# Performance work log

Measured on AMD Instinct MI355X. Metric: run time of the kernel, lower is better.

The kernel has to match this reference:

```python
import jax, jax.numpy as jnp
import numpy as np

N, K, D = 1000000, 4, 16

def setup_inputs() -> dict:
    key = jax.random.key(0)
    k1, k2, k3, k4, k5 = jax.random.split(key, 5)
    z = jax.random.normal(k1, (N, D), dtype=jnp.float32)
    phi = jax.nn.softmax(jax.random.normal(k2, (K,), dtype=jnp.float32))  # mixture weights, sum to 1
    mu = jax.random.normal(k3, (K, D), dtype=jnp.float32)
    # Upper-triangular Cholesky-like factor with positive diagonal (module calls
    # solve_triangular(..., upper=True), i.e. L is treated as upper triangular).
    A = jax.random.normal(k4, (K, D, D), dtype=jnp.float32) * 0.1
    diag = 0.8 + 0.4 * jax.random.uniform(k5, (K, D), dtype=jnp.float32)
    L = jnp.triu(A, 1) + jnp.zeros((K, D, D), jnp.float32).at[:, jnp.arange(D), jnp.arange(D)].set(diag)
    return {"z": z, "phi": phi, "mu": mu, "L": L}

def reference(z, phi, mu, L):
    # z: [N,D], phi: [K], mu: [K,D], L: [K,D,D] upper-triangular
    z_centered = z[:, None, :] - mu[None, :, :]            # [N,K,D]
    b = jnp.transpose(z_centered, (1, 2, 0))               # [K,D,N]
    v = jax.lax.linalg.triangular_solve(L, b, left_side=True, lower=False)  # [K,D,N]
    log_det_sigma = 2.0 * jnp.sum(jnp.log(jnp.diagonal(L, axis1=-2, axis2=-1)), axis=1)  # [K]
    d = z.shape[1]
    logits = jnp.log(phi)[:, None] - 0.5 * (
        jnp.sum(jnp.square(v), axis=1)                     # [K,N] Mahalanobis term
        + d * jnp.log(2.0 * jnp.pi)
        + log_det_sigma[:, None]
    )                                                      # [K,N]
    energies = -jax.scipy.special.logsumexp(logits, axis=0)  # [N]
    return energies
```

## Files before the change

### kernel.cpp

```cpp
#include <hip/hip_runtime.h>
#include <math.h>

namespace {

constexpr int KK = 4;
constexpr int DD = 16;
constexpr int BLOCK = 256;
constexpr int PTS = 4;
constexpr float LOG2PI = 1.8378770664093453f;
constexpr float INV_SQRT2 = 0.70710678118654752f;

__global__ __launch_bounds__(BLOCK, 4)
void gmm_energy(const float* __restrict__ z, const float* __restrict__ phi,
                const float* __restrict__ mu, const float* __restrict__ L,
                float* __restrict__ out, int N)
{
    __shared__ float sLinv[KK][DD][DD];
    __shared__ float sW[KK][DD];
    __shared__ float sC0[KK];

    const int tid = threadIdx.x;
    const int base = blockIdx.x * (BLOCK * PTS) + tid * PTS;

    float zr[PTS][DD];
    if (base + PTS <= N) {
        #pragma unroll
        for (int p = 0; p < PTS; ++p) {
            const float4* zp = reinterpret_cast<const float4*>(z + (size_t)(base + p) * DD);
            #pragma unroll
            for (int c = 0; c < 4; ++c) {
                float4 v = zp[c];
                zr[p][c * 4 + 0] = v.x;
                zr[p][c * 4 + 1] = v.y;
                zr[p][c * 4 + 2] = v.z;
                zr[p][c * 4 + 3] = v.w;
            }
        }
    } else {
        #pragma unroll
        for (int p = 0; p < PTS; ++p) {
            if (base + p < N) {
                const float4* zp = reinterpret_cast<const float4*>(z + (size_t)(base + p) * DD);
                #pragma unroll
                for (int c = 0; c < 4; ++c) {
                    float4 v = zp[c];
                    zr[p][c * 4 + 0] = v.x;
                    zr[p][c * 4 + 1] = v.y;
                    zr[p][c * 4 + 2] = v.z;
                    zr[p][c * 4 + 3] = v.w;
                }
            } else {
                #pragma unroll
                for (int d = 0; d < DD; ++d) zr[p][d] = 0.0f;
            }
        }
    }

    if (tid < KK * DD) {
        const int k = tid >> 4;
        const int j = tid & 15;
        const float* __restrict__ Lk = L + k * DD * DD;

        float rd[DD];
        #pragma unroll
        for (int i = 0; i < DD; ++i)
            rd[i] = __builtin_amdgcn_rcpf(Lk[i * DD + i]);

        float xv[DD];
        #pragma unroll
        for (int m = 0; m < DD; ++m) xv[m] = 0.0f;
        #pragma unroll
        for (int i = DD - 1; i >= 0; --i) {
            float s = (i == j) ? 1.0f : 0.0f;
            #pragma unroll
            for (int m = i + 1; m < DD; ++m)
                s = fmaf(-Lk[i * DD + m], xv[m], s);
            xv[i] = (i <= j) ? (s * rd[i]) : 0.0f;
        }
        #pragma unroll
        for (int i = 0; i < DD; ++i)
            sLinv[k][i][j] = xv[i] * INV_SQRT2;

        const int i2 = j;
        float w = 0.0f;
        #pragma unroll
        for (int jj = 0; jj < DD; ++jj)
            w = fmaf(sLinv[k][i2][jj], mu[k * DD + jj], w);
        sW[k][i2] = w;
    }
    if (tid < KK) {
        float logdet = 0.0f;
        #pragma unroll
        for (int i = 0; i < DD; ++i)
            logdet += __logf(L[tid * DD * DD + i * DD + i]);
        sC0[tid] = __logf(phi[tid]) - 8.0f * LOG2PI - logdet;
    }
    __syncthreads();

    float lg[PTS][KK];
    #pragma unroll
    for (int k = 0; k < KK; ++k) {
        float q[PTS];
        #pragma unroll
        for (int p = 0; p < PTS; ++p) q[p] = 0.0f;
        #pragma unroll
        for (int i = 0; i < DD; ++i) {
            const float wk = sW[k][i];
            const float cdiag = sLinv[k][i][i];
            float acc[PTS];
            #pragma unroll
            for (int p = 0; p < PTS; ++p)
                acc[p] = fmaf(cdiag, zr[p][i], -wk);
            #pragma unroll
            for (int j = i + 1; j < DD; ++j) {
                const float cf = sLinv[k][i][j];
                #pragma unroll
                for (int p = 0; p < PTS; ++p)
                    acc[p] = fmaf(cf, zr[p][j], acc[p]);
            }
            #pragma unroll
            for (int p = 0; p < PTS; ++p)
                q[p] = fmaf(acc[p], acc[p], q[p]);
        }
        const float c0 = sC0[k];
        #pragma unroll
        for (int p = 0; p < PTS; ++p)
            lg[p][k] = c0 - q[p];
    }

    float e[PTS];
    #pragma unroll
    for (int p = 0; p < PTS; ++p) {
        float m01 = fmaxf(lg[p][0], lg[p][1]);
        float m23 = fmaxf(lg[p][2], lg[p][3]);
        float m = fmaxf(m01, m23);
        float s = __expf(lg[p][0] - m) + __expf(lg[p][1] - m)
                + __expf(lg[p][2] - m) + __expf(lg[p][3] - m);
        e[p] = -(m + __logf(s));
    }

    if (base + PTS <= N) {
        float4 res;
        res.x = e[0]; res.y = e[1]; res.z = e[2]; res.w = e[3];
        *reinterpret_cast<float4*>(out + base) = res;
    } else {
        #pragma unroll
        for (int p = 0; p < PTS; ++p) {
            if (base + p < N) out[base + p] = e[p];
        }
    }
}

}

extern "C" void kernel_launch(void* const* d_in, const int* in_sizes, int n_in,
                              void* d_out, int out_size, void* d_ws, size_t ws_size,
                              hipStream_t stream) {
    const float* z   = (const float*)d_in[0];
    const float* phi = (const float*)d_in[1];
    const float* mu  = (const float*)d_in[2];
    const float* L   = (const float*)d_in[3];
    float* out = (float*)d_out;
    const int N = in_sizes[0] / DD;
    const int grid = (N + BLOCK * PTS - 1) / (BLOCK * PTS);
    gmm_energy<<<grid, BLOCK, 0, stream>>>(z, phi, mu, L, out, N);
}
```

Before: 115.8 us.

## Hoist per-component inverse Cholesky precompute into a separate prep kernel

Moves the triangular inverse, mean projection and constant-term computation out of every block into a single-block prep kernel that writes them to workspace. The main kernel then reads these coefficients from global memory with uniform addresses instead of LDS, drops the block barrier, and halves the points per thread to raise parallelism. This removes redundant per-block setup work and the sync stall. The cost is a second kernel launch and reliance on scalar/cached global loads for the coefficients.

```diff
diff --git a/kernel.cpp b/kernel.cpp
--- a/kernel.cpp
+++ b/kernel.cpp
@@ -6,24 +6,63 @@
 constexpr int KK = 4;
 constexpr int DD = 16;
 constexpr int BLOCK = 256;
-constexpr int PTS = 4;
+constexpr int PTS = 2;
 constexpr float LOG2PI = 1.8378770664093453f;
 constexpr float INV_SQRT2 = 0.70710678118654752f;
 
+constexpr int WOFF_W  = KK * DD * DD;
+constexpr int WOFF_C0 = WOFF_W + KK * DD;
+
+__global__ void gmm_prep(const float* __restrict__ phi, const float* __restrict__ mu,
+                         const float* __restrict__ L, float* __restrict__ ws)
+{
+    const int tid = threadIdx.x;
+    const int k = tid >> 4;
+    const int j = tid & 15;
+    const float* __restrict__ Lk = L + k * DD * DD;
+
+    float xv[DD];
+    #pragma unroll
+    for (int m = 0; m < DD; ++m) xv[m] = 0.0f;
+    #pragma unroll
+    for (int i = DD - 1; i >= 0; --i) {
+        float s = (i == j) ? 1.0f : 0.0f;
+        #pragma unroll
+        for (int m = i + 1; m < DD; ++m)
+            s = fmaf(-Lk[i * DD + m], xv[m], s);
+        xv[i] = (i <= j) ? (s / Lk[i * DD + i]) : 0.0f;
+    }
+    #pragma unroll
+    for (int i = 0; i < DD; ++i)
+        ws[k * DD * DD + i * DD + j] = xv[i] * INV_SQRT2;
+
+    __syncthreads();
+
+    float w = 0.0f;
+    #pragma unroll
+    for (int jj = 0; jj < DD; ++jj)
+        w = fmaf(ws[k * DD * DD + j * DD + jj], mu[k * DD + jj], w);
+    ws[WOFF_W + k * DD + j] = w;
+
+    if (tid < KK) {
+        float logdet = 0.0f;
+        #pragma unroll
+        for (int i = 0; i < DD; ++i)
+            logdet += __logf(L[tid * DD * DD + i * DD + i]);
+        ws[WOFF_C0 + tid] = __logf(phi[tid]) - 8.0f * LOG2PI - logdet;
+    }
+}
+
 __global__ __launch_bounds__(BLOCK, 4)
-void gmm_energy(const float* __restrict__ z, const float* __restrict__ phi,
-                const float* __restrict__ mu, const float* __restrict__ L,
+void gmm_energy(const float* __restrict__ z, const float* __restrict__ cw,
                 float* __restrict__ out, int N)
 {
-    __shared__ float sLinv[KK][DD][DD];
-    __shared__ float sW[KK][DD];
-    __shared__ float sC0[KK];
-
     const int tid = threadIdx.x;
     const int base = blockIdx.x * (BLOCK * PTS) + tid * PTS;
+    const bool full = (base + PTS <= N);
 
     float zr[PTS][DD];
-    if (base + PTS <= N) {
+    if (full) {
         #pragma unroll
         for (int p = 0; p < PTS; ++p) {
             const float4* zp = reinterpret_cast<const float4*>(z + (size_t)(base + p) * DD);
@@ -56,64 +95,24 @@
         }
     }
 
-    if (tid < KK * DD) {
-        const int k = tid >> 4;
-        const int j = tid & 15;
-        const float* __restrict__ Lk = L + k * DD * DD;
-
-        float rd[DD];
-        #pragma unroll
-        for (int i = 0; i < DD; ++i)
-            rd[i] = __builtin_amdgcn_rcpf(Lk[i * DD + i]);
-
-        float xv[DD];
-        #pragma unroll
-        for (int m = 0; m < DD; ++m) xv[m] = 0.0f;
-        #pragma unroll
-        for (int i = DD - 1; i >= 0; --i) {
-            float s = (i == j) ? 1.0f : 0.0f;
-            #pragma unroll
-            for (int m = i + 1; m < DD; ++m)
-                s = fmaf(-Lk[i * DD + m], xv[m], s);
-            xv[i] = (i <= j) ? (s * rd[i]) : 0.0f;
-        }
-        #pragma unroll
-        for (int i = 0; i < DD; ++i)
-            sLinv[k][i][j] = xv[i] * INV_SQRT2;
-
-        const int i2 = j;
-        float w = 0.0f;
-        #pragma unroll
-        for (int jj = 0; jj < DD; ++jj)
-            w = fmaf(sLinv[k][i2][jj], mu[k * DD + jj], w);
-        sW[k][i2] = w;
-    }
-    if (tid < KK) {
-        float logdet = 0.0f;
-        #pragma unroll
-        for (int i = 0; i < DD; ++i)
-            logdet += __logf(L[tid * DD * DD + i * DD + i]);
-        sC0[tid] = __logf(phi[tid]) - 8.0f * LOG2PI - logdet;
-    }
-    __syncthreads();
-
     float lg[PTS][KK];
     #pragma unroll
     for (int k = 0; k < KK; ++k) {
+        const float* __restrict__ Ck = cw + k * DD * DD;
+        const float* __restrict__ Wk = cw + WOFF_W + k * DD;
         float q[PTS];
         #pragma unroll
         for (int p = 0; p < PTS; ++p) q[p] = 0.0f;
         #pragma unroll
         for (int i = 0; i < DD; ++i) {
-            const float wk = sW[k][i];
-            const float cdiag = sLinv[k][i][i];
+            const float wk = Wk[i];
             float acc[PTS];
             #pragma unroll
             for (int p = 0; p < PTS; ++p)
-                acc[p] = fmaf(cdiag, zr[p][i], -wk);
+                acc[p] = fmaf(Ck[i * DD + i], zr[p][i], -wk);
             #pragma unroll
             for (int j = i + 1; j < DD; ++j) {
-                const float cf = sLinv[k][i][j];
+                const float cf = Ck[i * DD + j];
                 #pragma unroll
                 for (int p = 0; p < PTS; ++p)
                     acc[p] = fmaf(cf, zr[p][j], acc[p]);
@@ -122,7 +121,7 @@
             for (int p = 0; p < PTS; ++p)
                 q[p] = fmaf(acc[p], acc[p], q[p]);
         }
-        const float c0 = sC0[k];
+        const float c0 = cw[WOFF_C0 + k];
         #pragma unroll
         for (int p = 0; p < PTS; ++p)
             lg[p][k] = c0 - q[p];
@@ -139,10 +138,10 @@
         e[p] = -(m + __logf(s));
     }
 
-    if (base + PTS <= N) {
-        float4 res;
-        res.x = e[0]; res.y = e[1]; res.z = e[2]; res.w = e[3];
-        *reinterpret_cast<float4*>(out + base) = res;
+    if (full) {
+        float2 res;
+        res.x = e[0]; res.y = e[1];
+        *reinterpret_cast<float2*>(out + base) = res;
     } else {
         #pragma unroll
         for (int p = 0; p < PTS; ++p) {
@@ -161,7 +160,11 @@
     const float* mu  = (const float*)d_in[2];
     const float* L   = (const float*)d_in[3];
     float* out = (float*)d_out;
+    float* ws  = (float*)d_ws;
     const int N = in_sizes[0] / DD;
+
+    gmm_prep<<<1, 64, 0, stream>>>(phi, mu, L, ws);
+
     const int grid = (N + BLOCK * PTS - 1) / (BLOCK * PTS);
-    gmm_energy<<<grid, BLOCK, 0, stream>>>(z, phi, mu, L, out, N);
+    gmm_energy<<<grid, BLOCK, 0, stream>>>(z, ws, out, N);
 }
```

Result: no change. 113.7 us (-1.8%).
